# Performance work log

Measured on AMD Instinct MI355X. Metric: run time of the kernel, lower is better.

Reference implementation:

```python
import jax, jax.numpy as jnp
import numpy as np

LN_EPS = 1e-5


def setup_inputs() -> dict:
    key = jax.random.key(0)
    ks = jax.random.split(key, 10)
    B, T, D, K = 32, 1024, 512, 3
    enc = jax.random.normal(ks[0], (B, T, D), jnp.float32)
    dur = jax.random.randint(ks[1], (B, T), 0, 7, jnp.int32)
    s = 0.02
    return {
        "encoder_output": enc,
        "duration_target": dur,
        "conv1_w": jax.random.normal(ks[2], (K, D, D), jnp.float32) * s,  # HIO layout
        "conv1_b": jnp.zeros((D,), jnp.float32),
        "ln1_w": jnp.ones((D,), jnp.float32),
        "ln1_b": jnp.zeros((D,), jnp.float32),
        "conv2_w": jax.random.normal(ks[3], (K, D, D), jnp.float32) * s,
        "conv2_b": jnp.zeros((D,), jnp.float32),
        "ln2_w": jnp.ones((D,), jnp.float32),
        "ln2_b": jnp.zeros((D,), jnp.float32),
        "lin_w": jax.random.normal(ks[4], (D, 1), jnp.float32) * s,
        "lin_b": jnp.zeros((1,), jnp.float32),
        "max_len": 4096,
    }


def _conv_relu(x, w, b):
    # x: [B,T,D], w: [K, D_in, D_out] ('HIO'), 'SAME' padding == torch padding=1 for k=3
    y = jax.lax.conv_general_dilated(
        x, w, window_strides=(1,), padding="SAME",
        dimension_numbers=("NHC", "HIO", "NHC"))
    return jax.nn.relu(y + b)


def _layernorm(x, g, b):
    mu = jnp.mean(x, axis=-1, keepdims=True)
    var = jnp.mean(jnp.square(x - mu), axis=-1, keepdims=True)
    return (x - mu) * jax.lax.rsqrt(var + LN_EPS) * g + b


def reference(encoder_output, duration_target, conv1_w, conv1_b, ln1_w, ln1_b,
              conv2_w, conv2_b, ln2_w, ln2_b, lin_w, lin_b, max_len):
    B, T, D = encoder_output.shape
    # duration predictor: conv -> relu -> LN -> conv -> relu -> LN -> linear
    h = _layernorm(_conv_relu(encoder_output, conv1_w, conv1_b), ln1_w, ln1_b)
    h = _layernorm(_conv_relu(h, conv2_w, conv2_b), ln2_w, ln2_b)
    duration_predictor_output = (h @ lin_w + lin_b)[..., 0]  # [B,T]

    # training path: expand by duration_target via fused gather with cumulative offsets
    cum = jnp.cumsum(duration_target, axis=1)          # [B,T]
    pos = jnp.arange(max_len, dtype=jnp.int32)         # [L]
    # src index for output frame j: first t with cum[t] > j
    idx = jax.vmap(lambda c: jnp.searchsorted(c, pos, side="right"))(cum)  # [B,L]
    valid = pos[None, :] < cum[:, -1:]                  # [B,L]
    idx = jnp.minimum(idx, T - 1)
    expanded = jnp.take_along_axis(encoder_output, idx[:, :, None], axis=1)
    expanded = expanded * valid[:, :, None].astype(encoder_output.dtype)
    return expanded, duration_predictor_output
```

## Files before the change

### kernel.cpp

```cpp
#include <hip/hip_runtime.h>
#include <hip/hip_bf16.h>

#define BB 32
#define TT 1024
#define DD 512
#define LL 4096
#define KDIM 1536
#define TP 1026
#define ROWS (BB * TT)

typedef __attribute__((ext_vector_type(8))) short short8;
typedef __attribute__((ext_vector_type(8))) unsigned short ushort8;
typedef __attribute__((ext_vector_type(4))) float floatx4;

__device__ __forceinline__ unsigned short f2bf(float f) {
  unsigned int u = __builtin_bit_cast(unsigned int, f);
  u += 0x7FFF + ((u >> 16) & 1);
  return (unsigned short)(u >> 16);
}
__device__ __forceinline__ float bf2f(unsigned short h) {
  return __builtin_bit_cast(float, (unsigned int)h << 16);
}

#define GLOAD_LDS16(g, l)                                          \
  __builtin_amdgcn_global_load_lds(                                \
      (const __attribute__((address_space(1))) void*)(g),          \
      (__attribute__((address_space(3))) void*)(l), 16, 0, 0)

#define PAD_BLKS ((BB * TP) / 4)
__global__ __launch_bounds__(256) void pad_convert_kernel(
    const float* __restrict__ X, unsigned short* __restrict__ Xp,
    unsigned short* __restrict__ Hp) {
  const int lane = threadIdx.x & 63;
  if (blockIdx.x >= PAD_BLKS) {
    const int hid = (blockIdx.x - PAD_BLKS) * 4 + (threadIdx.x >> 6);
    const int b = hid >> 1;
    const long r = (long)b * TP + ((hid & 1) ? (TP - 1) : 0);
    *reinterpret_cast<ushort8*>(Hp + r * DD + lane * 8) = (ushort8)0;
    return;
  }
  const int row = blockIdx.x * 4 + (threadIdx.x >> 6);
  const int b  = row / TP;
  const int pr = row - b * TP;
  ushort8* o = reinterpret_cast<ushort8*>(Xp + (long)row * DD + lane * 8);
  ushort8 v;
  if (pr == 0 || pr == TP - 1) {
    v = (ushort8)0;
  } else {
    const float* p = X + ((long)(b * TT + pr - 1)) * DD + lane * 8;
    float4 a = *reinterpret_cast<const float4*>(p);
    float4 c = *reinterpret_cast<const float4*>(p + 4);
    v[0] = f2bf(a.x); v[1] = f2bf(a.y); v[2] = f2bf(a.z); v[3] = f2bf(a.w);
    v[4] = f2bf(c.x); v[5] = f2bf(c.y); v[6] = f2bf(c.z); v[7] = f2bf(c.w);
  }
  *o = v;
}

__global__ __launch_bounds__(256) void convert_wt_kernel(
    const float* __restrict__ W1, unsigned short* __restrict__ Wt1,
    const float* __restrict__ W2, unsigned short* __restrict__ Wt2) {
  __shared__ float tile[64][65];
  const float* W = (blockIdx.z == 0) ? W1 : W2;
  unsigned short* Wt = (blockIdx.z == 0) ? Wt1 : Wt2;
  const int n0 = blockIdx.x * 64;
  const int k0 = blockIdx.y * 64;
  const int c = threadIdx.x & 63;
  const int r4 = threadIdx.x >> 6;
#pragma unroll
  for (int r = 0; r < 16; ++r) tile[r * 4 + r4][c] = W[(long)(k0 + r * 4 + r4) * DD + n0 + c];
  __syncthreads();
#pragma unroll
  for (int r = 0; r < 16; ++r)
    Wt[(long)(n0 + r * 4 + r4) * KDIM + k0 + c] = f2bf(tile[c][r * 4 + r4]);
}

__global__ __launch_bounds__(256, 3) void conv_gemm_kernel(
    const unsigned short* __restrict__ Xp, const unsigned short* __restrict__ Wt,
    const float* __restrict__ bias, unsigned short* __restrict__ Ybf,
    float* __restrict__ Ps, float* __restrict__ Pq) {
  __shared__ unsigned short As[128 * 32];
  __shared__ unsigned short Bs[128 * 32];
  __shared__ float redS[2][128];
  __shared__ float redQ[2][128];

  const int tid  = threadIdx.x;
  const int wid  = tid >> 6;
  const int lane = tid & 63;
  const int m0   = blockIdx.x * 128;
  const int n0   = blockIdx.y * 128;
  const int wm   = (wid >> 1) * 64;
  const int wn   = (wid & 1) * 64;

  const int srow   = lane >> 2;
  const int gchunk = (lane & 3) ^ (srow & 3);
  const int frow   = lane & 15;
  const int quad   = lane >> 4;
  const int rdchunk = quad ^ (frow & 3);

  const int bA = m0 >> 10;
  const int t0 = m0 & (TT - 1);
  const unsigned short* gA0 =
      Xp + (long)(bA * TP + t0 + wid * 16 + srow) * DD + gchunk * 8;
  const unsigned short* gB0 =
      Wt + (long)(n0 + wid * 16 + srow) * KDIM + gchunk * 8;

  floatx4 acc[4][4];
#pragma unroll
  for (int i = 0; i < 4; ++i)
#pragma unroll
    for (int j = 0; j < 4; ++j) acc[i][j] = (floatx4){0.f, 0.f, 0.f, 0.f};

  for (int k0 = 0; k0 < KDIM; k0 += 32) {
    const int tap = k0 >> 9;
    const int c0  = k0 & 511;
    const unsigned short* gA = gA0 + (long)tap * DD + c0;
    GLOAD_LDS16(gA, &As[(wid * 16) * 32]);
    GLOAD_LDS16(gA + (long)64 * DD, &As[(64 + wid * 16) * 32]);
    GLOAD_LDS16(gB0 + k0, &Bs[(wid * 16) * 32]);
    GLOAD_LDS16(gB0 + (long)64 * KDIM + k0, &Bs[(64 + wid * 16) * 32]);
    __syncthreads();

    short8 af[4], bf[4];
#pragma unroll
    for (int i = 0; i < 4; ++i)
      af[i] = *reinterpret_cast<const short8*>(
          &As[(wm + i * 16 + frow) * 32 + rdchunk * 8]);
#pragma unroll
    for (int j = 0; j < 4; ++j)
      bf[j] = *reinterpret_cast<const short8*>(
          &Bs[(wn + j * 16 + frow) * 32 + rdchunk * 8]);
#pragma unroll
    for (int i = 0; i < 4; ++i)
#pragma unroll
      for (int j = 0; j < 4; ++j)
        acc[i][j] = __builtin_amdgcn_mfma_f32_16x16x32_bf16(
            af[i], bf[j], acc[i][j], 0, 0, 0);
    __syncthreads();
  }

  float bz[4];
#pragma unroll
  for (int j = 0; j < 4; ++j) bz[j] = bias[n0 + wn + j * 16 + frow];
  float ps[16], pq[16];
#pragma unroll
  for (int i = 0; i < 4; ++i)
#pragma unroll
    for (int r = 0; r < 4; ++r) {
      const long m = m0 + wm + i * 16 + quad * 4 + r;
      float s = 0.f, q = 0.f;
#pragma unroll
      for (int j = 0; j < 4; ++j) {
        const float v = fmaxf(acc[i][j][r] + bz[j], 0.f);
        Ybf[m * DD + n0 + wn + j * 16 + frow] = f2bf(v);
        s += v; q += v * v;
      }
      ps[i * 4 + r] = s; pq[i * 4 + r] = q;
    }
#pragma unroll
  for (int off = 1; off < 16; off <<= 1)
#pragma unroll
    for (int k = 0; k < 16; ++k) {
      ps[k] += __shfl_xor(ps[k], off);
      pq[k] += __shfl_xor(pq[k], off);
    }
  if (frow == 0) {
#pragma unroll
    for (int i = 0; i < 4; ++i)
#pragma unroll
      for (int r = 0; r < 4; ++r) {
        const int row = wm + i * 16 + quad * 4 + r;
        redS[wn >> 6][row] = ps[i * 4 + r];
        redQ[wn >> 6][row] = pq[i * 4 + r];
      }
  }
  __syncthreads();
  if (wn == 0 && frow == 0) {
    const long pb = (long)blockIdx.y * ROWS + m0;
#pragma unroll
    for (int i = 0; i < 4; ++i)
#pragma unroll
      for (int r = 0; r < 4; ++r) {
        const int row = wm + i * 16 + quad * 4 + r;
        Ps[pb + row] = redS[0][row] + redS[1][row];
        Pq[pb + row] = redQ[0][row] + redQ[1][row];
      }
  }
}

__global__ __launch_bounds__(256) void ln_apply1_kernel(
    const unsigned short* __restrict__ Ybf, const float* __restrict__ Ps,
    const float* __restrict__ Pq, const float* __restrict__ g,
    const float* __restrict__ be, unsigned short* __restrict__ Hp) {
  const int row  = blockIdx.x * 4 + (threadIdx.x >> 6);
  const int lane = threadIdx.x & 63;
  const float s = Ps[row] + Ps[ROWS + row] + Ps[2 * ROWS + row] + Ps[3 * ROWS + row];
  const float q = Pq[row] + Pq[ROWS + row] + Pq[2 * ROWS + row] + Pq[3 * ROWS + row];
  const float mu = s * (1.f / DD);
  const float var = q * (1.f / DD) - mu * mu;
  const float rs = rsqrtf(var + 1e-5f);
  ushort8 y = *reinterpret_cast<const ushort8*>(Ybf + (long)row * DD + lane * 8);
  float4 g0 = *reinterpret_cast<const float4*>(g + lane * 8);
  float4 g1 = *reinterpret_cast<const float4*>(g + lane * 8 + 4);
  float4 b0 = *reinterpret_cast<const float4*>(be + lane * 8);
  float4 b1 = *reinterpret_cast<const float4*>(be + lane * 8 + 4);
  ushort8 o;
  o[0] = f2bf((bf2f(y[0]) - mu) * rs * g0.x + b0.x);
  o[1] = f2bf((bf2f(y[1]) - mu) * rs * g0.y + b0.y);
  o[2] = f2bf((bf2f(y[2]) - mu) * rs * g0.z + b0.z);
  o[3] = f2bf((bf2f(y[3]) - mu) * rs * g0.w + b0.w);
  o[4] = f2bf((bf2f(y[4]) - mu) * rs * g1.x + b1.x);
  o[5] = f2bf((bf2f(y[5]) - mu) * rs * g1.y + b1.y);
  o[6] = f2bf((bf2f(y[6]) - mu) * rs * g1.z + b1.z);
  o[7] = f2bf((bf2f(y[7]) - mu) * rs * g1.w + b1.w);
  const int b = row >> 10, t = row & (TT - 1);
  *reinterpret_cast<ushort8*>(Hp + (long)(b * TP + t + 1) * DD + lane * 8) = o;
}

__global__ __launch_bounds__(256) void ln_apply2_kernel(
    const unsigned short* __restrict__ Ybf, const float* __restrict__ Ps,
    const float* __restrict__ Pq, const float* __restrict__ g,
    const float* __restrict__ be, const float* __restrict__ lw,
    const float* __restrict__ lb, float* __restrict__ outD) {
  const int row  = blockIdx.x * 4 + (threadIdx.x >> 6);
  const int lane = threadIdx.x & 63;
  const float s = Ps[row] + Ps[ROWS + row] + Ps[2 * ROWS + row] + Ps[3 * ROWS + row];
  const float q = Pq[row] + Pq[ROWS + row] + Pq[2 * ROWS + row] + Pq[3 * ROWS + row];
  const float mu = s * (1.f / DD);
  const float var = q * (1.f / DD) - mu * mu;
  const float rs = rsqrtf(var + 1e-5f);
  ushort8 y = *reinterpret_cast<const ushort8*>(Ybf + (long)row * DD + lane * 8);
  float4 g0 = *reinterpret_cast<const float4*>(g + lane * 8);
  float4 g1 = *reinterpret_cast<const float4*>(g + lane * 8 + 4);
  float4 b0 = *reinterpret_cast<const float4*>(be + lane * 8);
  float4 b1 = *reinterpret_cast<const float4*>(be + lane * 8 + 4);
  float4 w0 = *reinterpret_cast<const float4*>(lw + lane * 8);
  float4 w1 = *reinterpret_cast<const float4*>(lw + lane * 8 + 4);
  float d = ((bf2f(y[0]) - mu) * rs * g0.x + b0.x) * w0.x +
            ((bf2f(y[1]) - mu) * rs * g0.y + b0.y) * w0.y +
            ((bf2f(y[2]) - mu) * rs * g0.z + b0.z) * w0.z +
            ((bf2f(y[3]) - mu) * rs * g0.w + b0.w) * w0.w +
            ((bf2f(y[4]) - mu) * rs * g1.x + b1.x) * w1.x +
            ((bf2f(y[5]) - mu) * rs * g1.y + b1.y) * w1.y +
            ((bf2f(y[6]) - mu) * rs * g1.z + b1.z) * w1.z +
            ((bf2f(y[7]) - mu) * rs * g1.w + b1.w) * w1.w;
#pragma unroll
  for (int off = 32; off > 0; off >>= 1) d += __shfl_xor(d, off);
  if (lane == 0) outD[row] = d + lb[0];
}

__global__ __launch_bounds__(1024) void cumsum_kernel(
    const int* __restrict__ dur, int* __restrict__ cum) {
  __shared__ int s[TT];
  const int b = blockIdx.x, t = threadIdx.x;
  s[t] = dur[b * TT + t];
  __syncthreads();
  for (int off = 1; off < TT; off <<= 1) {
    int x = (t >= off) ? s[t - off] : 0;
    __syncthreads();
    s[t] += x;
    __syncthreads();
  }
  cum[b * TT + t] = s[t];
}

__global__ __launch_bounds__(128) void gather_kernel(
    const float* __restrict__ X, const int* __restrict__ cum,
    float* __restrict__ out) {
  const long blk = blockIdx.x;
  const int b = (int)(blk >> 12);
  const int j = (int)(blk & (LL - 1));
  const int* c = cum + b * TT;
  float4* o = reinterpret_cast<float4*>(out + blk * DD) + threadIdx.x;
  const int total = c[TT - 1];
  if (j >= total) {
    *o = make_float4(0.f, 0.f, 0.f, 0.f);
    return;
  }
  int lo = 0, hi = TT - 1;
  while (lo < hi) {
    const int mid = (lo + hi) >> 1;
    if (c[mid] <= j) lo = mid + 1; else hi = mid;
  }
  const float4* src =
      reinterpret_cast<const float4*>(X + ((long)b * TT + lo) * DD) +
      threadIdx.x;
  *o = *src;
}

extern "C" void kernel_launch(void* const* d_in, const int* in_sizes, int n_in,
                              void* d_out, int out_size, void* d_ws,
                              size_t ws_size, hipStream_t stream) {
  const float* enc = (const float*)d_in[0];
  const int* dur   = (const int*)d_in[1];
  const float* w1  = (const float*)d_in[2];
  const float* b1  = (const float*)d_in[3];
  const float* g1  = (const float*)d_in[4];
  const float* be1 = (const float*)d_in[5];
  const float* w2  = (const float*)d_in[6];
  const float* b2  = (const float*)d_in[7];
  const float* g2  = (const float*)d_in[8];
  const float* be2 = (const float*)d_in[9];
  const float* lw  = (const float*)d_in[10];
  const float* lb  = (const float*)d_in[11];

  float* out = (float*)d_out;
  float* expanded = out;
  float* dpo = out + (long)BB * LL * DD;

  unsigned short* enc_pad = (unsigned short*)(expanded);
  unsigned short* h1_pad  = (unsigned short*)(expanded + 9000000);
  unsigned short* wt1     = (unsigned short*)(expanded + 18000000);
  unsigned short* wt2     = (unsigned short*)(expanded + 18400000);
  unsigned short* ybf1    = (unsigned short*)(expanded + 19000000);
  unsigned short* ybf2    = (unsigned short*)(expanded + 27400000);
  float* p1s = expanded + 36000000;
  float* p1q = expanded + 36200000;
  float* p2s = expanded + 36400000;
  float* p2q = expanded + 36600000;
  int* cum = (int*)d_ws;

  pad_convert_kernel<<<PAD_BLKS + 16, 256, 0, stream>>>(enc, enc_pad, h1_pad);
  convert_wt_kernel<<<dim3(DD / 64, KDIM / 64, 2), 256, 0, stream>>>(
      w1, wt1, w2, wt2);

  dim3 gemm_grid(ROWS / 128, DD / 128);
  conv_gemm_kernel<<<gemm_grid, 256, 0, stream>>>(enc_pad, wt1, b1, ybf1,
                                                  p1s, p1q);
  ln_apply1_kernel<<<ROWS / 4, 256, 0, stream>>>(ybf1, p1s, p1q, g1, be1,
                                                 h1_pad);
  conv_gemm_kernel<<<gemm_grid, 256, 0, stream>>>(h1_pad, wt2, b2, ybf2,
                                                  p2s, p2q);
  ln_apply2_kernel<<<ROWS / 4, 256, 0, stream>>>(ybf2, p2s, p2q, g2, be2,
                                                 lw, lb, dpo);

  cumsum_kernel<<<BB, 1024, 0, stream>>>(dur, cum);
  gather_kernel<<<BB * LL, 128, 0, stream>>>(enc, cum, expanded);
}
```

Measured before the change: 533.0 us.

## Fuse conv GEMM with LayerNorm using full-width N tiles and double buffering

Each conv GEMM now computes a full 128x512 output row tile in a 512-thread block, so the LayerNorm statistics are finished inside the block and the normalization (plus the final linear projection for layer 2) is applied straight from the accumulators. This drops the bf16 intermediate Y buffers, the partial-sum arrays and the two separate ln_apply kernels. LDS staging is double-buffered so the next K slice is prefetched while MFMAs run. The trade-off is higher register pressure (a 4x8 accumulator tile per wave), more LDS per block, and a grid of only 256 blocks, which may leave CUs underused.

```diff
diff --git a/kernel.cpp b/kernel.cpp
--- a/kernel.cpp
+++ b/kernel.cpp
@@ -74,84 +74,103 @@
     Wt[(long)(n0 + r * 4 + r4) * KDIM + k0 + c] = f2bf(tile[c][r * 4 + r4]);
 }
 
-__global__ __launch_bounds__(256, 3) void conv_gemm_kernel(
+template <int LAYER>
+__global__ __launch_bounds__(512, 2) void fused_conv_ln_kernel(
     const unsigned short* __restrict__ Xp, const unsigned short* __restrict__ Wt,
-    const float* __restrict__ bias, unsigned short* __restrict__ Ybf,
-    float* __restrict__ Ps, float* __restrict__ Pq) {
-  __shared__ unsigned short As[128 * 32];
-  __shared__ unsigned short Bs[128 * 32];
-  __shared__ float redS[2][128];
-  __shared__ float redQ[2][128];
+    const float* __restrict__ bias, const float* __restrict__ g,
+    const float* __restrict__ be, const float* __restrict__ lw,
+    const float* __restrict__ lb, unsigned short* __restrict__ Hp,
+    float* __restrict__ dpo) {
+  __shared__ unsigned short As[2][128 * 32];
+  __shared__ unsigned short Bs[2][512 * 32];
+  __shared__ float sS[4][128];
+  __shared__ float sQ[4][128];
+  __shared__ float muL[128];
+  __shared__ float rsL[128];
 
   const int tid  = threadIdx.x;
+  const int lane = tid & 63;
   const int wid  = tid >> 6;
-  const int lane = tid & 63;
-  const int m0   = blockIdx.x * 128;
-  const int n0   = blockIdx.y * 128;
-  const int wm   = (wid >> 1) * 64;
-  const int wn   = (wid & 1) * 64;
-
-  const int srow   = lane >> 2;
+  const int srow = lane >> 2;
   const int gchunk = (lane & 3) ^ (srow & 3);
-  const int frow   = lane & 15;
-  const int quad   = lane >> 4;
-  const int rdchunk = quad ^ (frow & 3);
-
+  const int frow = lane & 15;
+  const int quad = lane >> 4;
+  const int rdch = quad ^ (frow & 3);
+  const int wm = (wid >> 2) * 64;
+  const int wn = (wid & 3) * 128;
+  const int wc = wid & 3;
+
+  const int m0 = blockIdx.x * 128;
   const int bA = m0 >> 10;
   const int t0 = m0 & (TT - 1);
+
   const unsigned short* gA0 =
       Xp + (long)(bA * TP + t0 + wid * 16 + srow) * DD + gchunk * 8;
   const unsigned short* gB0 =
-      Wt + (long)(n0 + wid * 16 + srow) * KDIM + gchunk * 8;
-
-  floatx4 acc[4][4];
+      Wt + (long)(wid * 16 + srow) * KDIM + gchunk * 8;
+
+  floatx4 acc[4][8];
 #pragma unroll
   for (int i = 0; i < 4; ++i)
 #pragma unroll
-    for (int j = 0; j < 4; ++j) acc[i][j] = (floatx4){0.f, 0.f, 0.f, 0.f};
-
+    for (int j = 0; j < 8; ++j) acc[i][j] = (floatx4){0.f, 0.f, 0.f, 0.f};
+
+#define STAGE(bi, kk)                                                         \
+  do {                                                                        \
+    const int tap_ = (kk) >> 9;                                               \
+    const int c0_  = (kk) & 511;                                              \
+    GLOAD_LDS16(gA0 + (long)tap_ * DD + c0_, &As[bi][(wid * 16) * 32]);       \
+    GLOAD_LDS16(gB0 + (kk),                   &Bs[bi][(wid * 16) * 32]);      \
+    GLOAD_LDS16(gB0 + (long)128 * KDIM + (kk), &Bs[bi][(128 + wid * 16) * 32]); \
+    GLOAD_LDS16(gB0 + (long)256 * KDIM + (kk), &Bs[bi][(256 + wid * 16) * 32]); \
+    GLOAD_LDS16(gB0 + (long)384 * KDIM + (kk), &Bs[bi][(384 + wid * 16) * 32]); \
+  } while (0)
+
+  STAGE(0, 0);
+  __syncthreads();
+  int cur = 0;
   for (int k0 = 0; k0 < KDIM; k0 += 32) {
-    const int tap = k0 >> 9;
-    const int c0  = k0 & 511;
-    const unsigned short* gA = gA0 + (long)tap * DD + c0;
-    GLOAD_LDS16(gA, &As[(wid * 16) * 32]);
-    GLOAD_LDS16(gA + (long)64 * DD, &As[(64 + wid * 16) * 32]);
-    GLOAD_LDS16(gB0 + k0, &Bs[(wid * 16) * 32]);
-    GLOAD_LDS16(gB0 + (long)64 * KDIM + k0, &Bs[(64 + wid * 16) * 32]);
+    if (k0 + 32 < KDIM) STAGE(cur ^ 1, k0 + 32);
+    short8 a_[4], b_[8];
+#pragma unroll
+    for (int i = 0; i < 4; ++i)
+      a_[i] = *reinterpret_cast<const short8*>(
+          &As[cur][(wm + i * 16 + frow) * 32 + rdch * 8]);
+#pragma unroll
+    for (int j = 0; j < 8; ++j)
+      b_[j] = *reinterpret_cast<const short8*>(
+          &Bs[cur][(wn + j * 16 + frow) * 32 + rdch * 8]);
+#pragma unroll
+    for (int i = 0; i < 4; ++i)
+#pragma unroll
+      for (int j = 0; j < 8; ++j)
+        acc[i][j] = __builtin_amdgcn_mfma_f32_16x16x32_bf16(
+            a_[i], b_[j], acc[i][j], 0, 0, 0);
     __syncthreads();
-
-    short8 af[4], bf[4];
-#pragma unroll
-    for (int i = 0; i < 4; ++i)
-      af[i] = *reinterpret_cast<const short8*>(
-          &As[(wm + i * 16 + frow) * 32 + rdchunk * 8]);
-#pragma unroll
-    for (int j = 0; j < 4; ++j)
-      bf[j] = *reinterpret_cast<const short8*>(
-          &Bs[(wn + j * 16 + frow) * 32 + rdchunk * 8]);
-#pragma unroll
-    for (int i = 0; i < 4; ++i)
-#pragma unroll
-      for (int j = 0; j < 4; ++j)
-        acc[i][j] = __builtin_amdgcn_mfma_f32_16x16x32_bf16(
-            af[i], bf[j], acc[i][j], 0, 0, 0);
-    __syncthreads();
-  }
-
-  float bz[4];
-#pragma unroll
-  for (int j = 0; j < 4; ++j) bz[j] = bias[n0 + wn + j * 16 + frow];
+    cur ^= 1;
+  }
+#undef STAGE
+
+  float bz[8];
+#pragma unroll
+  for (int j = 0; j < 8; ++j) bz[j] = bias[wn + j * 16 + frow];
+#pragma unroll
+  for (int i = 0; i < 4; ++i)
+#pragma unroll
+    for (int j = 0; j < 8; ++j)
+#pragma unroll
+      for (int r = 0; r < 4; ++r)
+        acc[i][j][r] = fmaxf(acc[i][j][r] + bz[j], 0.f);
+
   float ps[16], pq[16];
 #pragma unroll
   for (int i = 0; i < 4; ++i)
 #pragma unroll
     for (int r = 0; r < 4; ++r) {
-      const long m = m0 + wm + i * 16 + quad * 4 + r;
       float s = 0.f, q = 0.f;
 #pragma unroll
-      for (int j = 0; j < 4; ++j) {
-        const float v = fmaxf(acc[i][j][r] + bz[j], 0.f);
-        Ybf[m * DD + n0 + wn + j * 16 + frow] = f2bf(v);
+      for (int j = 0; j < 8; ++j) {
+        const float v = acc[i][j][r];
         s += v; q += v * v;
       }
       ps[i * 4 + r] = s; pq[i * 4 + r] = q;
@@ -169,83 +188,69 @@
 #pragma unroll
       for (int r = 0; r < 4; ++r) {
         const int row = wm + i * 16 + quad * 4 + r;
-        redS[wn >> 6][row] = ps[i * 4 + r];
-        redQ[wn >> 6][row] = pq[i * 4 + r];
+        sS[wc][row] = ps[i * 4 + r];
+        sQ[wc][row] = pq[i * 4 + r];
       }
   }
   __syncthreads();
-  if (wn == 0 && frow == 0) {
-    const long pb = (long)blockIdx.y * ROWS + m0;
+  if (tid < 128) {
+    const float s = sS[0][tid] + sS[1][tid] + sS[2][tid] + sS[3][tid];
+    const float q = sQ[0][tid] + sQ[1][tid] + sQ[2][tid] + sQ[3][tid];
+    const float mu = s * (1.f / DD);
+    const float var = q * (1.f / DD) - mu * mu;
+    muL[tid] = mu;
+    rsL[tid] = rsqrtf(var + 1e-5f);
+  }
+  __syncthreads();
+
+  float gg[8], bb[8];
+#pragma unroll
+  for (int j = 0; j < 8; ++j) {
+    gg[j] = g[wn + j * 16 + frow];
+    bb[j] = be[wn + j * 16 + frow];
+  }
+
+  if constexpr (LAYER == 1) {
 #pragma unroll
     for (int i = 0; i < 4; ++i)
 #pragma unroll
       for (int r = 0; r < 4; ++r) {
         const int row = wm + i * 16 + quad * 4 + r;
-        Ps[pb + row] = redS[0][row] + redS[1][row];
-        Pq[pb + row] = redQ[0][row] + redQ[1][row];
+        const float mu = muL[row];
+        const float rs = rsL[row];
+        const long orow = (long)(bA * TP + t0 + row + 1) * DD;
+#pragma unroll
+        for (int j = 0; j < 8; ++j) {
+          const float v = (acc[i][j][r] - mu) * rs * gg[j] + bb[j];
+          Hp[orow + wn + j * 16 + frow] = f2bf(v);
+        }
       }
-  }
-}
-
-__global__ __launch_bounds__(256) void ln_apply1_kernel(
-    const unsigned short* __restrict__ Ybf, const float* __restrict__ Ps,
-    const float* __restrict__ Pq, const float* __restrict__ g,
-    const float* __restrict__ be, unsigned short* __restrict__ Hp) {
-  const int row  = blockIdx.x * 4 + (threadIdx.x >> 6);
-  const int lane = threadIdx.x & 63;
-  const float s = Ps[row] + Ps[ROWS + row] + Ps[2 * ROWS + row] + Ps[3 * ROWS + row];
-  const float q = Pq[row] + Pq[ROWS + row] + Pq[2 * ROWS + row] + Pq[3 * ROWS + row];
-  const float mu = s * (1.f / DD);
-  const float var = q * (1.f / DD) - mu * mu;
-  const float rs = rsqrtf(var + 1e-5f);
-  ushort8 y = *reinterpret_cast<const ushort8*>(Ybf + (long)row * DD + lane * 8);
-  float4 g0 = *reinterpret_cast<const float4*>(g + lane * 8);
-  float4 g1 = *reinterpret_cast<const float4*>(g + lane * 8 + 4);
-  float4 b0 = *reinterpret_cast<const float4*>(be + lane * 8);
-  float4 b1 = *reinterpret_cast<const float4*>(be + lane * 8 + 4);
-  ushort8 o;
-  o[0] = f2bf((bf2f(y[0]) - mu) * rs * g0.x + b0.x);
-  o[1] = f2bf((bf2f(y[1]) - mu) * rs * g0.y + b0.y);
-  o[2] = f2bf((bf2f(y[2]) - mu) * rs * g0.z + b0.z);
-  o[3] = f2bf((bf2f(y[3]) - mu) * rs * g0.w + b0.w);
-  o[4] = f2bf((bf2f(y[4]) - mu) * rs * g1.x + b1.x);
-  o[5] = f2bf((bf2f(y[5]) - mu) * rs * g1.y + b1.y);
-  o[6] = f2bf((bf2f(y[6]) - mu) * rs * g1.z + b1.z);
-  o[7] = f2bf((bf2f(y[7]) - mu) * rs * g1.w + b1.w);
-  const int b = row >> 10, t = row & (TT - 1);
-  *reinterpret_cast<ushort8*>(Hp + (long)(b * TP + t + 1) * DD + lane * 8) = o;
-}
-
-__global__ __launch_bounds__(256) void ln_apply2_kernel(
-    const unsigned short* __restrict__ Ybf, const float* __restrict__ Ps,
-    const float* __restrict__ Pq, const float* __restrict__ g,
-    const float* __restrict__ be, const float* __restrict__ lw,
-    const float* __restrict__ lb, float* __restrict__ outD) {
-  const int row  = blockIdx.x * 4 + (threadIdx.x >> 6);
-  const int lane = threadIdx.x & 63;
-  const float s = Ps[row] + Ps[ROWS + row] + Ps[2 * ROWS + row] + Ps[3 * ROWS + row];
-  const float q = Pq[row] + Pq[ROWS + row] + Pq[2 * ROWS + row] + Pq[3 * ROWS + row];
-  const float mu = s * (1.f / DD);
-  const float var = q * (1.f / DD) - mu * mu;
-  const float rs = rsqrtf(var + 1e-5f);
-  ushort8 y = *reinterpret_cast<const ushort8*>(Ybf + (long)row * DD + lane * 8);
-  float4 g0 = *reinterpret_cast<const float4*>(g + lane * 8);
-  float4 g1 = *reinterpret_cast<const float4*>(g + lane * 8 + 4);
-  float4 b0 = *reinterpret_cast<const float4*>(be + lane * 8);
-  float4 b1 = *reinterpret_cast<const float4*>(be + lane * 8 + 4);
-  float4 w0 = *reinterpret_cast<const float4*>(lw + lane * 8);
-  float4 w1 = *reinterpret_cast<const float4*>(lw + lane * 8 + 4);
-  float d = ((bf2f(y[0]) - mu) * rs * g0.x + b0.x) * w0.x +
-            ((bf2f(y[1]) - mu) * rs * g0.y + b0.y) * w0.y +
-            ((bf2f(y[2]) - mu) * rs * g0.z + b0.z) * w0.z +
-            ((bf2f(y[3]) - mu) * rs * g0.w + b0.w) * w0.w +
-            ((bf2f(y[4]) - mu) * rs * g1.x + b1.x) * w1.x +
-            ((bf2f(y[5]) - mu) * rs * g1.y + b1.y) * w1.y +
-            ((bf2f(y[6]) - mu) * rs * g1.z + b1.z) * w1.z +
-            ((bf2f(y[7]) - mu) * rs * g1.w + b1.w) * w1.w;
-#pragma unroll
-  for (int off = 32; off > 0; off >>= 1) d += __shfl_xor(d, off);
-  if (lane == 0) outD[row] = d + lb[0];
+  } else {
+    float ww[8];
+#pragma unroll
+    for (int j = 0; j < 8; ++j) ww[j] = lw[wn + j * 16 + frow];
+#pragma unroll
+    for (int i = 0; i < 4; ++i)
+#pragma unroll
+      for (int r = 0; r < 4; ++r) {
+        const int row = wm + i * 16 + quad * 4 + r;
+        const float mu = muL[row];
+        const float rs = rsL[row];
+        float d = 0.f;
+#pragma unroll
+        for (int j = 0; j < 8; ++j) {
+          const float v = (acc[i][j][r] - mu) * rs * gg[j] + bb[j];
+          d += v * ww[j];
+        }
+#pragma unroll
+        for (int off = 1; off < 16; off <<= 1) d += __shfl_xor(d, off);
+        if (frow == 0) sS[wc][row] = d;
+      }
+    __syncthreads();
+    if (tid < 128)
+      dpo[m0 + tid] =
+          sS[0][tid] + sS[1][tid] + sS[2][tid] + sS[3][tid] + lb[0];
+  }
 }
 
 __global__ __launch_bounds__(1024) void cumsum_kernel(
@@ -311,27 +316,16 @@
   unsigned short* h1_pad  = (unsigned short*)(expanded + 9000000);
   unsigned short* wt1     = (unsigned short*)(expanded + 18000000);
   unsigned short* wt2     = (unsigned short*)(expanded + 18400000);
-  unsigned short* ybf1    = (unsigned short*)(expanded + 19000000);
-  unsigned short* ybf2    = (unsigned short*)(expanded + 27400000);
-  float* p1s = expanded + 36000000;
-  float* p1q = expanded + 36200000;
-  float* p2s = expanded + 36400000;
-  float* p2q = expanded + 36600000;
   int* cum = (int*)d_ws;
 
   pad_convert_kernel<<<PAD_BLKS + 16, 256, 0, stream>>>(enc, enc_pad, h1_pad);
   convert_wt_kernel<<<dim3(DD / 64, KDIM / 64, 2), 256, 0, stream>>>(
       w1, wt1, w2, wt2);
 
-  dim3 gemm_grid(ROWS / 128, DD / 128);
-  conv_gemm_kernel<<<gemm_grid, 256, 0, stream>>>(enc_pad, wt1, b1, ybf1,
-                                                  p1s, p1q);
-  ln_apply1_kernel<<<ROWS / 4, 256, 0, stream>>>(ybf1, p1s, p1q, g1, be1,
-                                                 h1_pad);
-  conv_gemm_kernel<<<gemm_grid, 256, 0, stream>>>(h1_pad, wt2, b2, ybf2,
-                                                  p2s, p2q);
-  ln_apply2_kernel<<<ROWS / 4, 256, 0, stream>>>(ybf2, p2s, p2q, g2, be2,
-                                                 lw, lb, dpo);
+  fused_conv_ln_kernel<1><<<ROWS / 128, 512, 0, stream>>>(
+      enc_pad, wt1, b1, g1, be1, nullptr, nullptr, h1_pad, nullptr);
+  fused_conv_ln_kernel<2><<<ROWS / 128, 512, 0, stream>>>(
+      h1_pad, wt2, b2, g2, be2, lw, lb, nullptr, dpo);
 
   cumsum_kernel<<<BB, 1024, 0, stream>>>(dur, cum);
   gather_kernel<<<BB * LL, 128, 0, stream>>>(enc, cum, expanded);
```

Result: no change. 524.3 us (-1.6%).
